# Performance work log

Measured on AMD Instinct MI355X. Metric: run time of the kernel, lower is better.

## Reference

```python
import jax, jax.numpy as jnp
import numpy as np

AGENT_RADIUS = 0.5
SAFETY_DIST = 0.1
QP_ITERS = 300


def _qp_solve(p, G, h):
    """Batched QP: min_u 0.5 u^T u + p^T u  s.t.  G u <= h  (Q = I).
    Solved in the dual by projected gradient ascent (differentiable, fixed iters).
    p: [B,2], G: [B,m,2], h: [B,m] -> u: [B,2]
    """
    GGt = jnp.einsum('bmi,bni->bmn', G, G)                 # [B,m,m]
    q = jnp.einsum('bmi,bi->bm', G, p) + h                 # [B,m]
    # Lipschitz upper bound per sample (Frobenius norm of GG^T)
    L = jnp.sqrt(jnp.sum(GGt * GGt, axis=(1, 2))) + 1e-6   # [B]
    alpha = (1.0 / L)[:, None]

    def step(lam, _):
        grad = jnp.einsum('bmn,bn->bm', GGt, lam) + q
        lam = jnp.maximum(lam - alpha * grad, 0.0)
        return lam, None

    lam0 = jnp.zeros_like(h)
    lam, _ = jax.lax.scan(step, lam0, None, length=QP_ITERS)
    u = -p - jnp.einsum('bmi,bm->bi', G, lam)
    return u


def setup_inputs() -> dict:
    key = jax.random.key(0)
    ks = jax.random.split(key, 20)
    B, F, H1, H2 = 8192, 8, 1024, 512

    def w(k, i, o):
        return (jax.random.normal(k, (i, o), jnp.float32) / np.sqrt(i)).astype(jnp.float32)

    obs_xy = jax.random.uniform(ks[17], (8, 2), jnp.float32, -10.0, 10.0)
    obs_r = jax.random.uniform(ks[18], (8, 1), jnp.float32, 0.3, 0.8)
    return {
        'x': jax.random.normal(ks[0], (B, F), jnp.float32),
        'mean': 0.1 * jax.random.normal(ks[1], (F,), jnp.float32),
        'std': jax.random.uniform(ks[2], (F,), jnp.float32, 0.5, 1.5),
        'W1': w(ks[3], F, H1), 'b1': jnp.zeros((H1,), jnp.float32),
        'W21': w(ks[4], H1, H2), 'b21': jnp.zeros((H2,), jnp.float32),
        'W22': w(ks[5], H1, H2), 'b22': jnp.zeros((H2,), jnp.float32),
        'W23': w(ks[6], H1, H2), 'b23': jnp.zeros((H2,), jnp.float32),
        'W31': w(ks[7], H2, 2), 'b31': jnp.zeros((2,), jnp.float32),
        'W32': w(ks[8], H2, 2), 'b32': jnp.zeros((2,), jnp.float32),
        'W33': w(ks[9], H2, 1), 'b33': jnp.zeros((1,), jnp.float32),
        'obstacles': jnp.concatenate([obs_xy, obs_r], axis=1),  # [8,3] (x,y,r)
        'sgn': 1,
    }


def reference(x, mean, std, W1, b1, W21, b21, W22, b22, W23, b23,
              W31, b31, W32, b32, W33, b33, obstacles, sgn):
    B = x.shape[0]
    x0 = x * std + mean                                   # un-normalized state [B,8]

    h1 = jax.nn.relu(x @ W1 + b1)
    x21 = jax.nn.relu(h1 @ W21 + b21)
    x22 = jax.nn.relu(h1 @ W22 + b22)
    x23 = jax.nn.relu(h1 @ W23 + b23)
    x31 = x21 @ W31 + b31                                 # QP linear term p [B,2]
    x32 = 4.0 * jax.nn.sigmoid(x22 @ W32 + b32)           # CBF gains p1,p2 [B,2]
    x33 = 4.0 * jax.nn.sigmoid(x23 @ W33 + b33)           # liveness gain (unused, smg off)

    px, py, theta, v = x0[:, 0], x0[:, 1], x0[:, 2], x0[:, 3]
    st, ct = jnp.sin(theta)[:, None], jnp.cos(theta)[:, None]
    vb = v[:, None]

    # static obstacles broadcast to batch + opponent as last obstacle -> [B, m]
    ox = jnp.concatenate([jnp.broadcast_to(obstacles[:, 0][None], (B, obstacles.shape[0])), x0[:, 4:5]], axis=1)
    oy = jnp.concatenate([jnp.broadcast_to(obstacles[:, 1][None], (B, obstacles.shape[0])), x0[:, 5:6]], axis=1)
    orad = jnp.concatenate([jnp.broadcast_to(obstacles[:, 2][None], (B, obstacles.shape[0])),
                            jnp.full((B, 1), AGENT_RADIUS, x0.dtype)], axis=1)

    R = AGENT_RADIUS + orad + SAFETY_DIST
    dx = px[:, None] - ox                                  # [B,m]
    dy = py[:, None] - oy

    barrier = dx * dx + dy * dy - R * R
    barrier_dot = 2.0 * dx * vb * ct + 2.0 * dy * vb * st
    Lf2b = (2.0 * v * v)[:, None]
    LgLfbu1 = -2.0 * dx * vb * st + 2.0 * dy * vb * ct
    LgLfbu2 = 2.0 * dx * ct + 2.0 * dy * st
    G = jnp.stack([-LgLfbu1, -LgLfbu2], axis=-1)           # [B,m,2]
    p1, p2 = x32[:, 0:1], x32[:, 1:2]
    h = Lf2b + (p1 + p2) * barrier_dot + p1 * p2 * barrier # [B,m]

    u = _qp_solve(x31, G, h)                               # [B,2]
    return u
```

## Files before the change

kernel.cpp:

```cpp
#include <hip/hip_runtime.h>
#include <cstdint>
#include <cstddef>

typedef unsigned short u16;
typedef u16   u16x8  __attribute__((ext_vector_type(8)));
typedef __bf16 bf16x8 __attribute__((ext_vector_type(8)));
typedef float f32x4  __attribute__((ext_vector_type(4)));

__device__ __forceinline__ float bf2f(u16 v) {
  unsigned int u = ((unsigned int)v) << 16;
  return __builtin_bit_cast(float, u);
}
__device__ __forceinline__ u16 f2bf(float f) {
  unsigned int x = __builtin_bit_cast(unsigned int, f);
  x += 0x7fffu + ((x >> 16) & 1u);
  return (u16)(x >> 16);
}

__global__ __launch_bounds__(256) void k_tr(const float* __restrict__ W21,
                                            const float* __restrict__ W22,
                                            u16* __restrict__ Wt) {
  __shared__ u16 s[64][65];
  const int b   = blockIdx.x;
  const int mat = b >> 7;
  const int tt  = b & 127;
  const int k0  = (tt >> 3) * 64;
  const int n0  = (tt & 7) * 64;
  const float* W = mat ? W22 : W21;
  const int tx = threadIdx.x & 63;
  const int ty = threadIdx.x >> 6;
#pragma unroll
  for (int i = 0; i < 16; ++i) {
    int r = i * 4 + ty;
    s[r][tx] = f2bf(W[(size_t)(k0 + r) * 512 + n0 + tx]);
  }
  __syncthreads();
  const int nbase = mat * 512 + n0;
#pragma unroll
  for (int i = 0; i < 16; ++i) {
    int r = i * 4 + ty;
    Wt[(size_t)(nbase + r) * 1024 + k0 + tx] = s[tx][r];
  }
}

__global__ __launch_bounds__(256) void k_h1(const float* __restrict__ x,
                                            const float* __restrict__ W1,
                                            const float* __restrict__ b1,
                                            u16* __restrict__ h1) {
  const int col = blockIdx.x * 256 + threadIdx.x;
  const int row = blockIdx.y;
  const f32x4* xp = (const f32x4*)(x + (size_t)row * 8);
  f32x4 xa = xp[0], xb = xp[1];
  float acc = b1[col];
#pragma unroll
  for (int f = 0; f < 4; ++f) {
    acc = fmaf(xa[f], W1[f * 1024 + col], acc);
    acc = fmaf(xb[f], W1[(f + 4) * 1024 + col], acc);
  }
  h1[(size_t)row * 1024 + col] = f2bf(fmaxf(acc, 0.f));
}

__global__ __launch_bounds__(256) void k_gemm(const u16* __restrict__ A,
                                              const u16* __restrict__ Bt,
                                              const float* __restrict__ b21,
                                              const float* __restrict__ b22,
                                              u16* __restrict__ X2) {
  constexpr int K = 1024;
  constexpr int BK = 32;
  __shared__ u16 As[128 * BK];
  __shared__ u16 Bs[128 * BK];

  const int t    = threadIdx.x;
  const int row0 = blockIdx.y * 128;
  const int col0 = blockIdx.x * 128;
  const int w    = t >> 6;
  const int lane = t & 63;
  const int wr   = w >> 1, wc = w & 1;
  const int lrow = lane & 15;
  const int lk   = (lane >> 4) * 8;

  f32x4 acc[4][4];
#pragma unroll
  for (int i = 0; i < 4; ++i)
#pragma unroll
    for (int j = 0; j < 4; ++j) acc[i][j] = f32x4{0.f, 0.f, 0.f, 0.f};

  u16x8 ld[4];
#pragma unroll
  for (int j = 0; j < 4; ++j) {
    int c = (j * 256 + t) & 511;
    const u16* base = (j < 2) ? (A + (size_t)(row0 + (c >> 2)) * K)
                              : (Bt + (size_t)(col0 + (c >> 2)) * K);
    ld[j] = *(const u16x8*)(base + (c & 3) * 8);
  }

  for (int kt = 0; kt < K / BK; ++kt) {
#pragma unroll
    for (int j = 0; j < 4; ++j) {
      int c = (j * 256 + t) & 511;
      u16* dst = (j < 2) ? (As + c * 8) : (Bs + c * 8);
      *(u16x8*)dst = ld[j];
    }
    __syncthreads();
    if (kt + 1 < K / BK) {
#pragma unroll
      for (int j = 0; j < 4; ++j) {
        int c = (j * 256 + t) & 511;
        const u16* base = (j < 2) ? (A + (size_t)(row0 + (c >> 2)) * K)
                                  : (Bt + (size_t)(col0 + (c >> 2)) * K);
        ld[j] = *(const u16x8*)(base + (size_t)(kt + 1) * BK + (c & 3) * 8);
      }
    }
    bf16x8 af[4], bfr[4];
#pragma unroll
    for (int i = 0; i < 4; ++i)
      af[i] = __builtin_bit_cast(bf16x8,
          *(const u16x8*)(As + (wr * 64 + i * 16 + lrow) * BK + lk));
#pragma unroll
    for (int j = 0; j < 4; ++j)
      bfr[j] = __builtin_bit_cast(bf16x8,
          *(const u16x8*)(Bs + (wc * 64 + j * 16 + lrow) * BK + lk));
#pragma unroll
    for (int i = 0; i < 4; ++i)
#pragma unroll
      for (int j = 0; j < 4; ++j)
        acc[i][j] = __builtin_amdgcn_mfma_f32_16x16x32_bf16(af[i], bfr[j], acc[i][j], 0, 0, 0);
    __syncthreads();
  }

#pragma unroll
  for (int j = 0; j < 4; ++j) {
    int col = col0 + wc * 64 + j * 16 + lrow;
    float bias = (col < 512) ? b21[col] : b22[col - 512];
#pragma unroll
    for (int i = 0; i < 4; ++i) {
      int rbase = row0 + wr * 64 + i * 16 + (lane >> 4) * 4;
#pragma unroll
      for (int rr = 0; rr < 4; ++rr) {
        float v = acc[i][j][rr] + bias;
        X2[(size_t)(rbase + rr) * 1024 + col] = f2bf(fmaxf(v, 0.f));
      }
    }
  }
}

__global__ __launch_bounds__(64) void k_qp(const float* __restrict__ x,
                                           const float* __restrict__ mean_,
                                           const float* __restrict__ std_,
                                           const u16* __restrict__ X2,
                                           const float* __restrict__ W31,
                                           const float* __restrict__ b31,
                                           const float* __restrict__ W32,
                                           const float* __restrict__ b32,
                                           const float* __restrict__ obstacles,
                                           float* __restrict__ out) {
  __shared__ float w31x[512], w31y[512], w32x[512], w32y[512];
  for (int i = threadIdx.x; i < 512; i += 64) {
    w31x[i] = W31[2 * i]; w31y[i] = W31[2 * i + 1];
    w32x[i] = W32[2 * i]; w32y[i] = W32[2 * i + 1];
  }
  __syncthreads();

  const int r = blockIdx.x * 64 + threadIdx.x;
  const u16x8* rowp = (const u16x8*)(X2 + (size_t)r * 1024);

  float a31x = 0.f, a31y = 0.f, a32x = 0.f, a32y = 0.f;
#pragma unroll 2
  for (int c = 0; c < 64; ++c) {
    u16x8 v = rowp[c];
#pragma unroll
    for (int e = 0; e < 8; ++e) {
      float f = bf2f(v[e]); int k = c * 8 + e;
      a31x = fmaf(f, w31x[k], a31x);
      a31y = fmaf(f, w31y[k], a31y);
    }
  }
#pragma unroll 2
  for (int c = 0; c < 64; ++c) {
    u16x8 v = rowp[64 + c];
#pragma unroll
    for (int e = 0; e < 8; ++e) {
      float f = bf2f(v[e]); int k = c * 8 + e;
      a32x = fmaf(f, w32x[k], a32x);
      a32y = fmaf(f, w32y[k], a32y);
    }
  }
  float p0  = a31x + b31[0];
  float p1v = a31y + b31[1];
  float pp1 = 4.f / (1.f + expf(-(a32x + b32[0])));
  float pp2 = 4.f / (1.f + expf(-(a32y + b32[1])));

  const f32x4* xp = (const f32x4*)(x + (size_t)r * 8);
  f32x4 xa = xp[0], xb = xp[1];
  float x0[6];
#pragma unroll
  for (int f = 0; f < 4; ++f) x0[f] = xa[f] * std_[f] + mean_[f];
  x0[4] = xb[0] * std_[4] + mean_[4];
  x0[5] = xb[1] * std_[5] + mean_[5];
  float px = x0[0], py = x0[1], th = x0[2], v = x0[3], ax = x0[4], ay = x0[5];
  float st = sinf(th), ct = cosf(th);
  float Lf2b = 2.f * v * v;

  float G0[9], G1[9], q[9];
  float s00 = 0.f, s01 = 0.f, s11 = 0.f;
#pragma unroll
  for (int m = 0; m < 9; ++m) {
    float ox, oy, orad;
    if (m < 8) {
      ox = obstacles[m * 3]; oy = obstacles[m * 3 + 1]; orad = obstacles[m * 3 + 2];
    } else { ox = ax; oy = ay; orad = 0.5f; }
    float R  = 0.6f + orad;
    float dx = px - ox, dy = py - oy;
    float bar  = dx * dx + dy * dy - R * R;
    float dct  = dx * ct + dy * st;
    float bdot = 2.f * v * dct;
    float g0 = 2.f * v * (dx * st - dy * ct);
    float g1 = -2.f * dct;
    float h  = Lf2b + (pp1 + pp2) * bdot + pp1 * pp2 * bar;
    G0[m] = g0; G1[m] = g1;
    q[m] = g0 * p0 + g1 * p1v + h;
    s00 += g0 * g0; s01 += g0 * g1; s11 += g1 * g1;
  }
  float L = sqrtf(s00 * s00 + 2.f * s01 * s01 + s11 * s11) + 1e-6f;
  float alpha = 1.f / L;

  float lam[9];
#pragma unroll
  for (int m = 0; m < 9; ++m) lam[m] = 0.f;
  for (int it = 0; it < 300; ++it) {
    float t0 = 0.f, t1 = 0.f;
#pragma unroll
    for (int m = 0; m < 9; ++m) { t0 = fmaf(G0[m], lam[m], t0); t1 = fmaf(G1[m], lam[m], t1); }
#pragma unroll
    for (int m = 0; m < 9; ++m) {
      float g = fmaf(G0[m], t0, fmaf(G1[m], t1, q[m]));
      lam[m] = fmaxf(fmaf(-alpha, g, lam[m]), 0.f);
    }
  }
  float u0 = -p0, u1 = -p1v;
#pragma unroll
  for (int m = 0; m < 9; ++m) { u0 = fmaf(-G0[m], lam[m], u0); u1 = fmaf(-G1[m], lam[m], u1); }
  out[2 * (size_t)r]     = u0;
  out[2 * (size_t)r + 1] = u1;
}

extern "C" void kernel_launch(void* const* d_in, const int* in_sizes, int n_in,
                              void* d_out, int out_size, void* d_ws, size_t ws_size,
                              hipStream_t stream) {
  const float* x    = (const float*)d_in[0];
  const float* mean_= (const float*)d_in[1];
  const float* std_ = (const float*)d_in[2];
  const float* W1   = (const float*)d_in[3];
  const float* b1   = (const float*)d_in[4];
  const float* W21  = (const float*)d_in[5];
  const float* b21  = (const float*)d_in[6];
  const float* W22  = (const float*)d_in[7];
  const float* b22  = (const float*)d_in[8];
  const float* W31  = (const float*)d_in[11];
  const float* b31  = (const float*)d_in[12];
  const float* W32  = (const float*)d_in[13];
  const float* b32  = (const float*)d_in[14];
  const float* obst = (const float*)d_in[17];
  float* out = (float*)d_out;

  char* ws = (char*)d_ws;
  u16* Wt = (u16*)ws;
  u16* h1 = (u16*)(ws + (size_t)(1 << 21));
  u16* X2 = (u16*)(ws + (size_t)(1 << 21) + (size_t)(1 << 24));

  k_tr  <<<256, 256, 0, stream>>>(W21, W22, Wt);
  k_h1  <<<dim3(4, 8192), 256, 0, stream>>>(x, W1, b1, h1);
  k_gemm<<<dim3(8, 64), 256, 0, stream>>>(h1, Wt, b21, b22, X2);
  k_qp  <<<128, 64, 0, stream>>>(x, mean_, std_, X2, W31, b31, W32, b32, obst, out);
}
```

Measured before the change: 186.9 us.

## Split output-head GEMV into wave-parallel kernel and use direct-to-LDS loads in GEMM

```diff
diff --git a/kernel.cpp b/kernel.cpp
--- a/kernel.cpp
+++ b/kernel.cpp
@@ -4,8 +4,10 @@
 
 typedef unsigned short u16;
 typedef u16   u16x8  __attribute__((ext_vector_type(8)));
+typedef u16   u16x4  __attribute__((ext_vector_type(4)));
 typedef __bf16 bf16x8 __attribute__((ext_vector_type(8)));
 typedef float f32x4  __attribute__((ext_vector_type(4)));
+typedef float f32x2  __attribute__((ext_vector_type(2)));
 
 __device__ __forceinline__ float bf2f(u16 v) {
   unsigned int u = ((unsigned int)v) << 16;
@@ -15,6 +17,12 @@
   unsigned int x = __builtin_bit_cast(unsigned int, f);
   x += 0x7fffu + ((x >> 16) & 1u);
   return (u16)(x >> 16);
+}
+
+__device__ __forceinline__ void gld_lds16(const u16* g, u16* l) {
+  __builtin_amdgcn_global_load_lds(
+      (const __attribute__((address_space(1))) unsigned int*)g,
+      (__attribute__((address_space(3))) unsigned int*)l, 16, 0, 0);
 }
 
 __global__ __launch_bounds__(256) void k_tr(const float* __restrict__ W21,
@@ -47,17 +55,21 @@
                                             const float* __restrict__ W1,
                                             const float* __restrict__ b1,
                                             u16* __restrict__ h1) {
-  const int col = blockIdx.x * 256 + threadIdx.x;
-  const int row = blockIdx.y;
-  const f32x4* xp = (const f32x4*)(x + (size_t)row * 8);
-  f32x4 xa = xp[0], xb = xp[1];
-  float acc = b1[col];
-#pragma unroll
-  for (int f = 0; f < 4; ++f) {
-    acc = fmaf(xa[f], W1[f * 1024 + col], acc);
-    acc = fmaf(xb[f], W1[(f + 4) * 1024 + col], acc);
-  }
-  h1[(size_t)row * 1024 + col] = f2bf(fmaxf(acc, 0.f));
+  const int row = blockIdx.x;
+  const int c4  = threadIdx.x * 4;
+  const float* xr = x + (size_t)row * 8;
+  f32x4 acc = *(const f32x4*)(b1 + c4);
+#pragma unroll
+  for (int f = 0; f < 8; ++f) {
+    float xv = xr[f];
+    f32x4 wv = *(const f32x4*)(W1 + f * 1024 + c4);
+#pragma unroll
+    for (int e = 0; e < 4; ++e) acc[e] = fmaf(xv, wv[e], acc[e]);
+  }
+  u16x4 o;
+#pragma unroll
+  for (int e = 0; e < 4; ++e) o[e] = f2bf(fmaxf(acc[e], 0.f));
+  *(u16x4*)(h1 + (size_t)row * 1024 + c4) = o;
 }
 
 __global__ __launch_bounds__(256) void k_gemm(const u16* __restrict__ A,
@@ -79,38 +91,31 @@
   const int lrow = lane & 15;
   const int lk   = (lane >> 4) * 8;
 
+  const int cA0 = t, cA1 = 256 + t;
+  const int cB0 = t, cB1 = 256 + t;
+  const u16* gA0 = A  + (size_t)(row0 + (cA0 >> 2)) * K + (cA0 & 3) * 8;
+  const u16* gA1 = A  + (size_t)(row0 + (cA1 >> 2)) * K + (cA1 & 3) * 8;
+  const u16* gB0 = Bt + (size_t)(col0 + (cB0 >> 2)) * K + (cB0 & 3) * 8;
+  const u16* gB1 = Bt + (size_t)(col0 + (cB1 >> 2)) * K + (cB1 & 3) * 8;
+  u16* lA0 = As + cA0 * 8;
+  u16* lA1 = As + cA1 * 8;
+  u16* lB0 = Bs + cB0 * 8;
+  u16* lB1 = Bs + cB1 * 8;
+
   f32x4 acc[4][4];
 #pragma unroll
   for (int i = 0; i < 4; ++i)
 #pragma unroll
     for (int j = 0; j < 4; ++j) acc[i][j] = f32x4{0.f, 0.f, 0.f, 0.f};
 
-  u16x8 ld[4];
-#pragma unroll
-  for (int j = 0; j < 4; ++j) {
-    int c = (j * 256 + t) & 511;
-    const u16* base = (j < 2) ? (A + (size_t)(row0 + (c >> 2)) * K)
-                              : (Bt + (size_t)(col0 + (c >> 2)) * K);
-    ld[j] = *(const u16x8*)(base + (c & 3) * 8);
-  }
-
   for (int kt = 0; kt < K / BK; ++kt) {
-#pragma unroll
-    for (int j = 0; j < 4; ++j) {
-      int c = (j * 256 + t) & 511;
-      u16* dst = (j < 2) ? (As + c * 8) : (Bs + c * 8);
-      *(u16x8*)dst = ld[j];
-    }
+    gld_lds16(gA0, lA0);
+    gld_lds16(gA1, lA1);
+    gld_lds16(gB0, lB0);
+    gld_lds16(gB1, lB1);
+    gA0 += BK; gA1 += BK; gB0 += BK; gB1 += BK;
     __syncthreads();
-    if (kt + 1 < K / BK) {
-#pragma unroll
-      for (int j = 0; j < 4; ++j) {
-        int c = (j * 256 + t) & 511;
-        const u16* base = (j < 2) ? (A + (size_t)(row0 + (c >> 2)) * K)
-                                  : (Bt + (size_t)(col0 + (c >> 2)) * K);
-        ld[j] = *(const u16x8*)(base + (size_t)(kt + 1) * BK + (c & 3) * 8);
-      }
-    }
+
     bf16x8 af[4], bfr[4];
 #pragma unroll
     for (int i = 0; i < 4; ++i)
@@ -144,60 +149,66 @@
   }
 }
 
+__global__ __launch_bounds__(256) void k_head(const u16* __restrict__ X2,
+                                              const float* __restrict__ W31,
+                                              const float* __restrict__ W32,
+                                              float* __restrict__ head) {
+  const int wv   = threadIdx.x >> 6;
+  const int lane = threadIdx.x & 63;
+  const int r    = blockIdx.x * 4 + wv;
+  const u16* row = X2 + (size_t)r * 1024;
+
+  u16x8 v0 = *(const u16x8*)(row + lane * 8);
+  u16x8 v1 = *(const u16x8*)(row + 512 + lane * 8);
+  const f32x4* w31p = (const f32x4*)(W31 + lane * 16);
+  const f32x4* w32p = (const f32x4*)(W32 + lane * 16);
+
+  float a0x = 0.f, a0y = 0.f, a1x = 0.f, a1y = 0.f;
+#pragma unroll
+  for (int i = 0; i < 4; ++i) {
+    f32x4 wa = w31p[i];
+    float e0 = bf2f(v0[2 * i]), e1 = bf2f(v0[2 * i + 1]);
+    a0x = fmaf(e0, wa[0], a0x); a0y = fmaf(e0, wa[1], a0y);
+    a0x = fmaf(e1, wa[2], a0x); a0y = fmaf(e1, wa[3], a0y);
+    f32x4 wb = w32p[i];
+    float f0 = bf2f(v1[2 * i]), f1 = bf2f(v1[2 * i + 1]);
+    a1x = fmaf(f0, wb[0], a1x); a1y = fmaf(f0, wb[1], a1y);
+    a1x = fmaf(f1, wb[2], a1x); a1y = fmaf(f1, wb[3], a1y);
+  }
+#pragma unroll
+  for (int m = 32; m >= 1; m >>= 1) {
+    a0x += __shfl_xor(a0x, m, 64);
+    a0y += __shfl_xor(a0y, m, 64);
+    a1x += __shfl_xor(a1x, m, 64);
+    a1y += __shfl_xor(a1y, m, 64);
+  }
+  if (lane == 0)
+    *(f32x4*)(head + 4 * (size_t)r) = f32x4{a0x, a0y, a1x, a1y};
+}
+
 __global__ __launch_bounds__(64) void k_qp(const float* __restrict__ x,
                                            const float* __restrict__ mean_,
                                            const float* __restrict__ std_,
-                                           const u16* __restrict__ X2,
-                                           const float* __restrict__ W31,
+                                           const float* __restrict__ head,
                                            const float* __restrict__ b31,
-                                           const float* __restrict__ W32,
                                            const float* __restrict__ b32,
                                            const float* __restrict__ obstacles,
                                            float* __restrict__ out) {
-  __shared__ float w31x[512], w31y[512], w32x[512], w32y[512];
-  for (int i = threadIdx.x; i < 512; i += 64) {
-    w31x[i] = W31[2 * i]; w31y[i] = W31[2 * i + 1];
-    w32x[i] = W32[2 * i]; w32y[i] = W32[2 * i + 1];
-  }
-  __syncthreads();
-
   const int r = blockIdx.x * 64 + threadIdx.x;
-  const u16x8* rowp = (const u16x8*)(X2 + (size_t)r * 1024);
-
-  float a31x = 0.f, a31y = 0.f, a32x = 0.f, a32y = 0.f;
-#pragma unroll 2
-  for (int c = 0; c < 64; ++c) {
-    u16x8 v = rowp[c];
-#pragma unroll
-    for (int e = 0; e < 8; ++e) {
-      float f = bf2f(v[e]); int k = c * 8 + e;
-      a31x = fmaf(f, w31x[k], a31x);
-      a31y = fmaf(f, w31y[k], a31y);
-    }
-  }
-#pragma unroll 2
-  for (int c = 0; c < 64; ++c) {
-    u16x8 v = rowp[64 + c];
-#pragma unroll
-    for (int e = 0; e < 8; ++e) {
-      float f = bf2f(v[e]); int k = c * 8 + e;
-      a32x = fmaf(f, w32x[k], a32x);
-      a32y = fmaf(f, w32y[k], a32y);
-    }
-  }
-  float p0  = a31x + b31[0];
-  float p1v = a31y + b31[1];
-  float pp1 = 4.f / (1.f + expf(-(a32x + b32[0])));
-  float pp2 = 4.f / (1.f + expf(-(a32y + b32[1])));
+  f32x4 hd = *(const f32x4*)(head + 4 * (size_t)r);
+  float p0  = hd[0] + b31[0];
+  float p1v = hd[1] + b31[1];
+  float pp1 = 4.f / (1.f + expf(-(hd[2] + b32[0])));
+  float pp2 = 4.f / (1.f + expf(-(hd[3] + b32[1])));
 
   const f32x4* xp = (const f32x4*)(x + (size_t)r * 8);
   f32x4 xa = xp[0], xb = xp[1];
-  float x0[6];
-#pragma unroll
-  for (int f = 0; f < 4; ++f) x0[f] = xa[f] * std_[f] + mean_[f];
-  x0[4] = xb[0] * std_[4] + mean_[4];
-  x0[5] = xb[1] * std_[5] + mean_[5];
-  float px = x0[0], py = x0[1], th = x0[2], v = x0[3], ax = x0[4], ay = x0[5];
+  float px = xa[0] * std_[0] + mean_[0];
+  float py = xa[1] * std_[1] + mean_[1];
+  float th = xa[2] * std_[2] + mean_[2];
+  float v  = xa[3] * std_[3] + mean_[3];
+  float ax = xb[0] * std_[4] + mean_[4];
+  float ay = xb[1] * std_[5] + mean_[5];
   float st = sinf(th), ct = cosf(th);
   float Lf2b = 2.f * v * v;
 
@@ -228,9 +239,13 @@
 #pragma unroll
   for (int m = 0; m < 9; ++m) lam[m] = 0.f;
   for (int it = 0; it < 300; ++it) {
-    float t0 = 0.f, t1 = 0.f;
-#pragma unroll
-    for (int m = 0; m < 9; ++m) { t0 = fmaf(G0[m], lam[m], t0); t1 = fmaf(G1[m], lam[m], t1); }
+    float pr0[9], pr1[9];
+#pragma unroll
+    for (int m = 0; m < 9; ++m) { pr0[m] = G0[m] * lam[m]; pr1[m] = G1[m] * lam[m]; }
+    float t0 = (((pr0[0] + pr0[1]) + (pr0[2] + pr0[3])) +
+                ((pr0[4] + pr0[5]) + (pr0[6] + pr0[7]))) + pr0[8];
+    float t1 = (((pr1[0] + pr1[1]) + (pr1[2] + pr1[3])) +
+                ((pr1[4] + pr1[5]) + (pr1[6] + pr1[7]))) + pr1[8];
 #pragma unroll
     for (int m = 0; m < 9; ++m) {
       float g = fmaf(G0[m], t0, fmaf(G1[m], t1, q[m]));
@@ -240,8 +255,7 @@
   float u0 = -p0, u1 = -p1v;
 #pragma unroll
   for (int m = 0; m < 9; ++m) { u0 = fmaf(-G0[m], lam[m], u0); u1 = fmaf(-G1[m], lam[m], u1); }
-  out[2 * (size_t)r]     = u0;
-  out[2 * (size_t)r + 1] = u1;
+  *(f32x2*)(out + 2 * (size_t)r) = f32x2{u0, u1};
 }
 
 extern "C" void kernel_launch(void* const* d_in, const int* in_sizes, int n_in,
@@ -264,12 +278,14 @@
   float* out = (float*)d_out;
 
   char* ws = (char*)d_ws;
-  u16* Wt = (u16*)ws;
-  u16* h1 = (u16*)(ws + (size_t)(1 << 21));
-  u16* X2 = (u16*)(ws + (size_t)(1 << 21) + (size_t)(1 << 24));
+  u16*   Wt   = (u16*)ws;
+  u16*   h1   = (u16*)(ws + (size_t)(1 << 21));
+  u16*   X2   = (u16*)(ws + (size_t)(1 << 21) + (size_t)(1 << 24));
+  float* head = (float*)(ws + (size_t)(1 << 21) + 2 * (size_t)(1 << 24));
 
   k_tr  <<<256, 256, 0, stream>>>(W21, W22, Wt);
-  k_h1  <<<dim3(4, 8192), 256, 0, stream>>>(x, W1, b1, h1);
+  k_h1  <<<8192, 256, 0, stream>>>(x, W1, b1, h1);
   k_gemm<<<dim3(8, 64), 256, 0, stream>>>(h1, Wt, b21, b22, X2);
-  k_qp  <<<128, 64, 0, stream>>>(x, mean_, std_, X2, W31, b31, W32, b32, obst, out);
-}
+  k_head<<<2048, 256, 0, stream>>>(X2, W31, W32, head);
+  k_qp  <<<128, 64, 0, stream>>>(x, mean_, std_, head, b31, b32, obst, out);
+}
```

Result: faster. 172.5 us (-7.7%).
